# Kernel optimization log

Hardware: AMD Instinct MI355X
Metric: run time of the kernel (lower is better)

Reference implementation:

```python
import jax, jax.numpy as jnp
import numpy as np

N_NODES = 100000
N_EDGES = 1000000
D_IN = 64
D_HID = 64
D_OUT = 64


def setup_inputs() -> dict:
    key = jax.random.key(0)
    ks = jax.random.split(key, 8)
    x = jax.random.normal(ks[0], (N_NODES, D_IN), dtype=jnp.float32)
    edge_index = jax.random.randint(ks[1], (2, N_EDGES), 0, N_NODES, dtype=jnp.int64)
    s = 1.0 / np.sqrt(D_IN)
    # SAGEConv layer 1: lin_l (applied to aggregated neighbors, with bias), lin_r (root, no bias)
    W1l = jax.random.uniform(ks[2], (D_HID, D_IN), jnp.float32, -s, s)
    b1l = jnp.zeros((D_HID,), jnp.float32)
    W1r = jax.random.uniform(ks[3], (D_HID, D_IN), jnp.float32, -s, s)
    s2 = 1.0 / np.sqrt(D_HID)
    W2l = jax.random.uniform(ks[4], (D_OUT, D_HID), jnp.float32, -s2, s2)
    b2l = jnp.zeros((D_OUT,), jnp.float32)
    W2r = jax.random.uniform(ks[5], (D_OUT, D_HID), jnp.float32, -s2, s2)
    return {"x": x, "edge_index": edge_index,
            "W1l": W1l, "b1l": b1l, "W1r": W1r,
            "W2l": W2l, "b2l": b2l, "W2r": W2r}


def _sage_conv(x, src, dst, Wl, bl, Wr):
    # mean-aggregate neighbor features (messages flow src -> dst)
    msg_sum = jax.ops.segment_sum(x[src], dst, num_segments=N_NODES)  # [N, d]
    deg = jax.ops.segment_sum(jnp.ones((src.shape[0],), x.dtype), dst, num_segments=N_NODES)
    agg = msg_sum / jnp.maximum(deg, 1.0)[:, None]
    return agg @ Wl.T + bl + x @ Wr.T


def reference(x, edge_index, W1l, b1l, W1r, W2l, b2l, W2r):
    src, dst = edge_index[0], edge_index[1]
    h = _sage_conv(x, src, dst, W1l, b1l, W1r)
    h = jax.nn.relu(h)
    # dropout is identity in eval mode
    out = _sage_conv(h, src, dst, W2l, b2l, W2r)
    return out
```

## Files before the change

### kernel.cpp

```cpp
#include <hip/hip_runtime.h>

#define D 64
#define BK_SHIFT 8
#define BK_MASK 255
#define SEGCAP 4096
#define ESLICE 4096

typedef __attribute__((ext_vector_type(8))) short short8;
typedef __attribute__((ext_vector_type(4))) float floatx4;

__device__ __forceinline__ ushort f2bf(float f) {
    unsigned u = __float_as_uint(f);
    u += 0x7fffu + ((u >> 16) & 1u);
    return (ushort)(u >> 16);
}
__device__ __forceinline__ float bf2f(ushort h) {
    return __int_as_float(((unsigned)h) << 16);
}

__global__ void cast_kernel(const float* __restrict__ x, ushort* __restrict__ xh,
                            int* __restrict__ bkcnt, int* __restrict__ hist,
                            int* __restrict__ bincur0, int n4) {
    int i = blockIdx.x * blockDim.x + threadIdx.x;
    if (i < 512) bkcnt[i] = 0;
    if (i < 64) { hist[i] = 0; bincur0[i] = 0; }
    if (i >= n4) return;
    float4 v = ((const float4*)x)[i];
    ushort4 r;
    r.x = f2bf(v.x); r.y = f2bf(v.y); r.z = f2bf(v.z); r.w = f2bf(v.w);
    ((ushort4*)xh)[i] = r;
}

__global__ void bkcount_kernel(const int* __restrict__ ei, int* __restrict__ bkcnt,
                               int E, int B) {
    __shared__ int h[512];
    int tid = threadIdx.x;
    h[tid] = 0; h[tid + 256] = 0;
    __syncthreads();
    int e0 = blockIdx.x * ESLICE;
#pragma unroll 4
    for (int it = 0; it < ESLICE / 256; ++it) {
        int e = e0 + it * 256 + tid;
        if (e < E) atomicAdd(&h[ei[E + e] >> BK_SHIFT], 1);
    }
    __syncthreads();
    if (tid < B && h[tid]) atomicAdd(&bkcnt[tid], h[tid]);
    int t2 = tid + 256;
    if (t2 < B && h[t2]) atomicAdd(&bkcnt[t2], h[t2]);
}

__global__ void bkscan_kernel(const int* __restrict__ bkcnt, int* __restrict__ bkbeg,
                              int* __restrict__ bkcur, int B) {
    __shared__ int wsum[8];
    int tid = threadIdx.x;
    int lane = tid & 63, w = tid >> 6;
    int c = (tid < B) ? bkcnt[tid] : 0;
    int p = c;
#pragma unroll
    for (int o = 1; o < 64; o <<= 1) {
        int u = __shfl_up(p, o, 64);
        if (lane >= o) p += u;
    }
    if (lane == 63) wsum[w] = p;
    __syncthreads();
    int base = 0;
    for (int ww = 0; ww < w; ++ww) base += wsum[ww];
    int excl = base + p - c;
    if (tid < B) { bkbeg[tid] = excl; bkcur[tid] = excl; }
    if (tid == B - 1) bkbeg[B] = excl + c;
}

__global__ void route_kernel(const int* __restrict__ ei, int* __restrict__ bkcur,
                             int* __restrict__ bucketed, int E, int B) {
    __shared__ int h[512];
    __shared__ int gb[512];
    int tid = threadIdx.x;
    h[tid] = 0; h[tid + 256] = 0;
    __syncthreads();
    int e0 = blockIdx.x * ESLICE;
#pragma unroll 4
    for (int it = 0; it < ESLICE / 256; ++it) {
        int e = e0 + it * 256 + tid;
        if (e < E) atomicAdd(&h[ei[E + e] >> BK_SHIFT], 1);
    }
    __syncthreads();
    if (tid < B) gb[tid] = h[tid] ? atomicAdd(&bkcur[tid], h[tid]) : 0;
    int t2 = tid + 256;
    if (t2 < B) gb[t2] = h[t2] ? atomicAdd(&bkcur[t2], h[t2]) : 0;
    __syncthreads();
    h[tid] = 0; h[tid + 256] = 0;
    __syncthreads();
#pragma unroll 4
    for (int it = 0; it < ESLICE / 256; ++it) {
        int e = e0 + it * 256 + tid;
        if (e < E) {
            int dst = ei[E + e];
            int key = dst >> BK_SHIFT;
            int src = ei[e];
            int r = atomicAdd(&h[key], 1);
            bucketed[gb[key] + r] = (src << BK_SHIFT) | (dst & BK_MASK);
        }
    }
}

__global__ void csr_kernel(const int* __restrict__ bucketed, const int* __restrict__ bkbeg,
                           int* __restrict__ srclist, int* __restrict__ beg,
                           int* __restrict__ cnt, int* __restrict__ hist, int N) {
    __shared__ int lcnt[256];
    __shared__ int lbeg[256];
    __shared__ int seg[SEGCAP];
    __shared__ int wsum[4];
    __shared__ int lh[64];
    int k = blockIdx.x;
    int tid = threadIdx.x;
    int nd0 = k << BK_SHIFT;
    int nn = min(256, N - nd0);
    int ebeg = bkbeg[k], eend = bkbeg[k + 1];
    int ecnt = eend - ebeg;
    lcnt[tid] = 0;
    if (tid < 64) lh[tid] = 0;
    __syncthreads();
    for (int e = ebeg + tid; e < eend; e += 256)
        atomicAdd(&lcnt[bucketed[e] & BK_MASK], 1);
    __syncthreads();
    int c = lcnt[tid];
    int lane = tid & 63, w = tid >> 6;
    int p = c;
#pragma unroll
    for (int o = 1; o < 64; o <<= 1) {
        int u = __shfl_up(p, o, 64);
        if (lane >= o) p += u;
    }
    if (lane == 63) wsum[w] = p;
    __syncthreads();
    int base = 0;
    for (int ww = 0; ww < w; ++ww) base += wsum[ww];
    int excl = base + p - c;
    lbeg[tid] = excl;
    lcnt[tid] = 0;
    __syncthreads();
    if (ecnt <= SEGCAP) {
        for (int e = ebeg + tid; e < eend; e += 256) {
            int v = bucketed[e];
            int key = v & BK_MASK;
            int pos = lbeg[key] + atomicAdd(&lcnt[key], 1);
            seg[pos] = v >> BK_SHIFT;
        }
        __syncthreads();
        for (int i = tid; i < ecnt; i += 256)
            srclist[ebeg + i] = seg[i];
    } else {
        for (int e = ebeg + tid; e < eend; e += 256) {
            int v = bucketed[e];
            int key = v & BK_MASK;
            int pos = lbeg[key] + atomicAdd(&lcnt[key], 1);
            srclist[ebeg + pos] = v >> BK_SHIFT;
        }
    }
    __syncthreads();
    if (tid < nn) {
        int dg = lcnt[tid];
        cnt[nd0 + tid] = dg;
        beg[nd0 + tid] = ebeg + lbeg[tid];
        atomicAdd(&lh[dg < 63 ? dg : 63], 1);
    }
    __syncthreads();
    if (tid < 64 && lh[tid]) atomicAdd(&hist[tid], lh[tid]);
}

__global__ void scatter_kernel(const int* __restrict__ cnt, const int* __restrict__ hist,
                               int* __restrict__ bincur0, int* __restrict__ perm, int N) {
    __shared__ int lh[64];
    __shared__ int lbase[64];
    __shared__ int sbase[64];
    int tid = threadIdx.x;
    if (tid < 64) {
        lh[tid] = 0;
        int c = hist[tid];
        int p = c;
#pragma unroll
        for (int o = 1; o < 64; o <<= 1) {
            int u = __shfl_up(p, o, 64);
            if (tid >= o) p += u;
        }
        sbase[tid] = N - p;
    }
    __syncthreads();
    int i = blockIdx.x * blockDim.x + tid;
    int bin = 0, slot = 0;
    if (i < N) {
        int c = cnt[i];
        bin = c < 63 ? c : 63;
        slot = atomicAdd(&lh[bin], 1);
    }
    __syncthreads();
    if (tid < 64 && lh[tid] > 0) lbase[tid] = sbase[tid] + atomicAdd(&bincur0[tid], lh[tid]);
    __syncthreads();
    if (i < N) perm[lbase[bin] + slot] = i;
}


__global__ void __launch_bounds__(256, 4) sage_kernel(
    const ushort* __restrict__ inh,
    const int* __restrict__ perm,
    const int* __restrict__ beg_, const int* __restrict__ cnt_,
    const int* __restrict__ srclist,
    const float* __restrict__ Wl, const float* __restrict__ bl,
    const float* __restrict__ Wr,
    float* __restrict__ out_f32,
    ushort* __restrict__ out_bf,
    int N, int relu) {
    __shared__ short8 fL[8][64];
    __shared__ short8 fR[8][64];
    __shared__ float ot[4][16 * 68];
    int tid = threadIdx.x;
    int lane = tid & 63;
    {
        int c = tid >> 6;
        int n = lane & 15;
        int q = lane >> 4;
#pragma unroll
        for (int s = 0; s < 2; ++s) {
            const float* pl = Wl + (c * 16 + n) * D + s * 32 + q * 8;
            const float* pr = Wr + (c * 16 + n) * D + s * 32 + q * 8;
            short8 vl, vr;
#pragma unroll
            for (int j = 0; j < 8; ++j) {
                vl[j] = (short)f2bf(pl[j]);
                vr[j] = (short)f2bf(pr[j]);
            }
            fL[c * 2 + s][lane] = vl;
            fR[c * 2 + s][lane] = vr;
        }
    }
    __syncthreads();

    int m = lane & 15;
    int q = lane >> 4;
    float* otw = &ot[tid >> 6][0];
    float b0 = bl[m], b1 = bl[16 + m], b2 = bl[32 + m], b3 = bl[48 + m];
    int gwave   = blockIdx.x * 4 + (tid >> 6);
    int nwaves  = gridDim.x * 4;
    int ngroups = (N + 15) >> 4;

    for (int g = gwave; g < ngroups; g += nwaves) {
        int base = g * 16;
        bool nv = (base + m) < N;
        int node = nv ? perm[base + m] : 0;
        int beg = nv ? beg_[node] : 0;
        int deg = nv ? cnt_[node] : 0;

        int md = deg;
        md = max(md, __shfl_xor(md, 1, 64));
        md = max(md, __shfl_xor(md, 2, 64));
        md = max(md, __shfl_xor(md, 4, 64));
        md = max(md, __shfl_xor(md, 8, 64));

        float f0[8], f1[8];
#pragma unroll
        for (int u = 0; u < 8; ++u) { f0[u] = 0.f; f1[u] = 0.f; }

#pragma unroll 8
        for (int j = 0; j < md; ++j) {
            int idx = beg + ((j < deg) ? j : 0);
            int si = srclist[idx];
            const ushort* rp = inh + (size_t)si * D;
            short8 lo = *(const short8*)(rp + q * 8);
            short8 hi = *(const short8*)(rp + 32 + q * 8);
            float msk = (j < deg) ? 1.f : 0.f;
#pragma unroll
            for (int u = 0; u < 8; ++u) {
                f0[u] = fmaf(msk, bf2f((ushort)lo[u]), f0[u]);
                f1[u] = fmaf(msk, bf2f((ushort)hi[u]), f1[u]);
            }
        }

        float scale = (deg > 0) ? 1.0f / (float)deg : 0.0f;
        short8 a0, a1;
#pragma unroll
        for (int u = 0; u < 8; ++u) {
            a0[u] = (short)f2bf(f0[u] * scale);
            a1[u] = (short)f2bf(f1[u] * scale);
        }

        const ushort* rr = inh + (size_t)node * D;
        short8 r0 = *(const short8*)(rr + q * 8);
        short8 r1 = *(const short8*)(rr + 32 + q * 8);

#pragma unroll
        for (int c = 0; c < 4; ++c) {
            float bc = (c == 0) ? b0 : (c == 1) ? b1 : (c == 2) ? b2 : b3;
            floatx4 acc = {bc, bc, bc, bc};
            acc = __builtin_amdgcn_mfma_f32_16x16x32_bf16(a0, fL[c * 2 + 0][lane], acc, 0, 0, 0);
            acc = __builtin_amdgcn_mfma_f32_16x16x32_bf16(a1, fL[c * 2 + 1][lane], acc, 0, 0, 0);
            acc = __builtin_amdgcn_mfma_f32_16x16x32_bf16(r0, fR[c * 2 + 0][lane], acc, 0, 0, 0);
            acc = __builtin_amdgcn_mfma_f32_16x16x32_bf16(r1, fR[c * 2 + 1][lane], acc, 0, 0, 0);
#pragma unroll
            for (int r = 0; r < 4; ++r) {
                float v = acc[r];
                if (relu) v = fmaxf(v, 0.f);
                otw[(q * 4 + r) * 68 + c * 16 + m] = v;
            }
        }

        int rho = lane >> 2;
        int q4  = lane & 3;
        int onode = __shfl(node, rho, 64);
        const float* sp = &otw[rho * 68 + q4 * 16];
        if (base + rho < N) {
            if (out_bf) {
                uint u[8];
#pragma unroll
                for (int j = 0; j < 8; ++j)
                    u[j] = (uint)f2bf(sp[2 * j]) | ((uint)f2bf(sp[2 * j + 1]) << 16);
                uint4* dp = (uint4*)(out_bf + (size_t)onode * D + q4 * 16);
                uint4 w0 = {u[0], u[1], u[2], u[3]};
                uint4 w1 = {u[4], u[5], u[6], u[7]};
                dp[0] = w0; dp[1] = w1;
            } else {
                float4* dp = (float4*)(out_f32 + (size_t)onode * D + q4 * 16);
                const float4* s4 = (const float4*)sp;
                dp[0] = s4[0]; dp[1] = s4[1]; dp[2] = s4[2]; dp[3] = s4[3];
            }
        }
    }
}

extern "C" void kernel_launch(void* const* d_in, const int* in_sizes, int n_in,
                              void* d_out, int out_size, void* d_ws, size_t ws_size,
                              hipStream_t stream) {
    const float* x   = (const float*)d_in[0];
    const int*   ei  = (const int*)d_in[1];
    const float* W1l = (const float*)d_in[2];
    const float* b1l = (const float*)d_in[3];
    const float* W1r = (const float*)d_in[4];
    const float* W2l = (const float*)d_in[5];
    const float* b2l = (const float*)d_in[6];
    const float* W2r = (const float*)d_in[7];
    float* out = (float*)d_out;

    int N = in_sizes[0] / D;
    int E = in_sizes[1] / 2;
    int B = (N + BK_MASK) >> BK_SHIFT;

    char* ws = (char*)d_ws;
    ushort* xh = (ushort*)ws;
    ushort* hh = xh + (size_t)N * D;
    int*   bucketed = (int*)hh;
    int*   srclist  = (int*)(ws + (size_t)2 * N * D * 2);
    int*   beg      = srclist + E + 64;
    int*   cnt      = beg + N;
    int*   perm     = cnt + N;
    int*   hist     = perm + N;
    int*   bincur0  = hist + 64;
    int*   bkcnt    = bincur0 + 64;
    int*   bkbeg    = bkcnt + 512;
    int*   bkcur    = bkbeg + 513;

    int n4 = N * D / 4;
    cast_kernel<<<(n4 + 255) / 256, 256, 0, stream>>>(x, xh, bkcnt, hist, bincur0, n4);

    int nblocks = (N + 255) / 256;
    int eslices = (E + ESLICE - 1) / ESLICE;
    bkcount_kernel<<<eslices, 256, 0, stream>>>(ei, bkcnt, E, B);
    bkscan_kernel<<<1, 512, 0, stream>>>(bkcnt, bkbeg, bkcur, B);
    route_kernel<<<eslices, 256, 0, stream>>>(ei, bkcur, bucketed, E, B);
    csr_kernel<<<B, 256, 0, stream>>>(bucketed, bkbeg, srclist, beg, cnt, hist, N);
    scatter_kernel<<<nblocks, 256, 0, stream>>>(cnt, hist, bincur0, perm, N);

    int ngroups = (N + 15) / 16;
    int sblocks = (ngroups + 3) / 4;
    if (sblocks > 1024) sblocks = 1024;
    sage_kernel<<<sblocks, 256, 0, stream>>>(xh, perm, beg, cnt, srclist,
                                             W1l, b1l, W1r, nullptr, hh, N, 1);
    sage_kernel<<<sblocks, 256, 0, stream>>>(hh, perm, beg, cnt, srclist,
                                             W2l, b2l, W2r, out, nullptr, N, 0);
}
```

Measured before the change: 224.4 us.

## Fuse cast with bucket count, batch neighbor gathers by four, uncap sage grid

The bf16 cast and the destination-bucket histogram now run as one launch split by block index, and counter zeroing moves to a memset. The neighbor aggregation loop loads four source indices and their feature rows before accumulating, so more gathers are in flight per wave. The sage kernel grid is no longer capped at 1024 blocks and gets one block per four node groups. Together these aim to cut launch overhead and hide gather latency, at the cost of more registers and masked wasted loads when degrees are not multiples of four.

```diff
diff --git a/kernel.cpp b/kernel.cpp
--- a/kernel.cpp
+++ b/kernel.cpp
@@ -18,26 +18,24 @@
     return __int_as_float(((unsigned)h) << 16);
 }
 
-__global__ void cast_kernel(const float* __restrict__ x, ushort* __restrict__ xh,
-                            int* __restrict__ bkcnt, int* __restrict__ hist,
-                            int* __restrict__ bincur0, int n4) {
-    int i = blockIdx.x * blockDim.x + threadIdx.x;
-    if (i < 512) bkcnt[i] = 0;
-    if (i < 64) { hist[i] = 0; bincur0[i] = 0; }
-    if (i >= n4) return;
-    float4 v = ((const float4*)x)[i];
-    ushort4 r;
-    r.x = f2bf(v.x); r.y = f2bf(v.y); r.z = f2bf(v.z); r.w = f2bf(v.w);
-    ((ushort4*)xh)[i] = r;
-}
-
-__global__ void bkcount_kernel(const int* __restrict__ ei, int* __restrict__ bkcnt,
-                               int E, int B) {
+__global__ void cast_bkcount_kernel(const float* __restrict__ x, ushort* __restrict__ xh,
+                                    const int* __restrict__ ei, int* __restrict__ bkcnt,
+                                    int n4, int E, int B, int castb) {
+    int bid = blockIdx.x;
+    int tid = threadIdx.x;
+    if (bid < castb) {
+        int i = bid * 256 + tid;
+        if (i >= n4) return;
+        float4 v = ((const float4*)x)[i];
+        ushort4 r;
+        r.x = f2bf(v.x); r.y = f2bf(v.y); r.z = f2bf(v.z); r.w = f2bf(v.w);
+        ((ushort4*)xh)[i] = r;
+        return;
+    }
     __shared__ int h[512];
-    int tid = threadIdx.x;
     h[tid] = 0; h[tid + 256] = 0;
     __syncthreads();
-    int e0 = blockIdx.x * ESLICE;
+    int e0 = (bid - castb) * ESLICE;
 #pragma unroll 4
     for (int it = 0; it < ESLICE / 256; ++it) {
         int e = e0 + it * 256 + tid;
@@ -260,18 +258,42 @@
 #pragma unroll
         for (int u = 0; u < 8; ++u) { f0[u] = 0.f; f1[u] = 0.f; }
 
-#pragma unroll 8
-        for (int j = 0; j < md; ++j) {
-            int idx = beg + ((j < deg) ? j : 0);
-            int si = srclist[idx];
-            const ushort* rp = inh + (size_t)si * D;
-            short8 lo = *(const short8*)(rp + q * 8);
-            short8 hi = *(const short8*)(rp + 32 + q * 8);
-            float msk = (j < deg) ? 1.f : 0.f;
+        for (int j = 0; j < md; j += 4) {
+            int si0, si1, si2, si3;
+            {
+                int j0 = j,     i0 = beg + ((j0 < deg) ? j0 : 0);
+                int j1 = j + 1, i1 = beg + ((j1 < deg) ? j1 : 0);
+                int j2 = j + 2, i2 = beg + ((j2 < deg) ? j2 : 0);
+                int j3 = j + 3, i3 = beg + ((j3 < deg) ? j3 : 0);
+                si0 = srclist[i0]; si1 = srclist[i1];
+                si2 = srclist[i2]; si3 = srclist[i3];
+            }
+            const ushort* rp0 = inh + (size_t)si0 * D;
+            const ushort* rp1 = inh + (size_t)si1 * D;
+            const ushort* rp2 = inh + (size_t)si2 * D;
+            const ushort* rp3 = inh + (size_t)si3 * D;
+            short8 lo0 = *(const short8*)(rp0 + q * 8);
+            short8 hi0 = *(const short8*)(rp0 + 32 + q * 8);
+            short8 lo1 = *(const short8*)(rp1 + q * 8);
+            short8 hi1 = *(const short8*)(rp1 + 32 + q * 8);
+            short8 lo2 = *(const short8*)(rp2 + q * 8);
+            short8 hi2 = *(const short8*)(rp2 + 32 + q * 8);
+            short8 lo3 = *(const short8*)(rp3 + q * 8);
+            short8 hi3 = *(const short8*)(rp3 + 32 + q * 8);
+            float m0 = (j     < deg) ? 1.f : 0.f;
+            float m1 = (j + 1 < deg) ? 1.f : 0.f;
+            float m2 = (j + 2 < deg) ? 1.f : 0.f;
+            float m3 = (j + 3 < deg) ? 1.f : 0.f;
 #pragma unroll
             for (int u = 0; u < 8; ++u) {
-                f0[u] = fmaf(msk, bf2f((ushort)lo[u]), f0[u]);
-                f1[u] = fmaf(msk, bf2f((ushort)hi[u]), f1[u]);
+                f0[u] = fmaf(m0, bf2f((ushort)lo0[u]), f0[u]);
+                f1[u] = fmaf(m0, bf2f((ushort)hi0[u]), f1[u]);
+                f0[u] = fmaf(m1, bf2f((ushort)lo1[u]), f0[u]);
+                f1[u] = fmaf(m1, bf2f((ushort)hi1[u]), f1[u]);
+                f0[u] = fmaf(m2, bf2f((ushort)lo2[u]), f0[u]);
+                f1[u] = fmaf(m2, bf2f((ushort)hi2[u]), f1[u]);
+                f0[u] = fmaf(m3, bf2f((ushort)lo3[u]), f0[u]);
+                f1[u] = fmaf(m3, bf2f((ushort)hi3[u]), f1[u]);
             }
         }
 
@@ -357,20 +379,21 @@
     int*   bkbeg    = bkcnt + 512;
     int*   bkcur    = bkbeg + 513;
 
+    (void)hipMemsetAsync(hist, 0, (64 + 64 + 512) * sizeof(int), stream);
+
     int n4 = N * D / 4;
-    cast_kernel<<<(n4 + 255) / 256, 256, 0, stream>>>(x, xh, bkcnt, hist, bincur0, n4);
-
-    int nblocks = (N + 255) / 256;
+    int castb = (n4 + 255) / 256;
     int eslices = (E + ESLICE - 1) / ESLICE;
-    bkcount_kernel<<<eslices, 256, 0, stream>>>(ei, bkcnt, E, B);
+    cast_bkcount_kernel<<<castb + eslices, 256, 0, stream>>>(x, xh, ei, bkcnt,
+                                                             n4, E, B, castb);
     bkscan_kernel<<<1, 512, 0, stream>>>(bkcnt, bkbeg, bkcur, B);
     route_kernel<<<eslices, 256, 0, stream>>>(ei, bkcur, bucketed, E, B);
     csr_kernel<<<B, 256, 0, stream>>>(bucketed, bkbeg, srclist, beg, cnt, hist, N);
+    int nblocks = (N + 255) / 256;
     scatter_kernel<<<nblocks, 256, 0, stream>>>(cnt, hist, bincur0, perm, N);
 
     int ngroups = (N + 15) / 16;
     int sblocks = (ngroups + 3) / 4;
-    if (sblocks > 1024) sblocks = 1024;
     sage_kernel<<<sblocks, 256, 0, stream>>>(xh, perm, beg, cnt, srclist,
                                              W1l, b1l, W1r, nullptr, hh, N, 1);
     sage_kernel<<<sblocks, 256, 0, stream>>>(hh, perm, beg, cnt, srclist,
```

Result: slower. 248.6 us (+10.8%).
